# Performance work log

Measured on AMD Instinct MI355X. Metric: run time of the kernel, lower is better.

## Reference

```python
import jax, jax.numpy as jnp
import numpy as np

B, N, T, C = 16, 12, 128, 128  # batch, num_classes (nodes), temporal, channels


def _bn(x, gamma, beta, eps=1e-5):
    # BatchNorm2d in training mode: stats over (batch, t, c), channel axis 1, biased var
    mean = jnp.mean(x, axis=(0, 2, 3), keepdims=True)
    var = jnp.var(x, axis=(0, 2, 3), keepdims=True)
    xn = (x - mean) * jax.lax.rsqrt(var + eps)
    return xn * gamma[None, :, None, None] + beta[None, :, None, None]


def setup_inputs() -> dict:
    key = jax.random.key(0)
    ks = jax.random.split(key, 3)
    scale = np.float32(np.sqrt(2.0 / C))
    inp = {
        'x': jax.random.normal(ks[0], (B, N, T, C), dtype=jnp.float32),
        'edge': jax.random.normal(ks[1], (B, N * N, T, C), dtype=jnp.float32),
    }
    wk = jax.random.split(ks[2], 10)
    for name, k in zip(['A1', 'B1', 'E1', 'U1', 'V1', 'A2', 'B2', 'E2', 'U2', 'V2'], wk):
        inp[name] = jax.random.normal(k, (C, C), dtype=jnp.float32) * scale
    for name, dim in [('g_e1', N * N), ('b_e1', N * N), ('g_v1', N), ('b_v1', N),
                      ('g_e2', N * N), ('b_e2', N * N), ('g_v2', N), ('b_v2', N)]:
        inp[name] = jnp.ones((dim,), jnp.float32) if name[0] == 'g' else jnp.zeros((dim,), jnp.float32)
    return inp


def _forward(x, edge, A1, B1, E1, U1, V1, A2, B2, E2, U2, V2,
             g_e1, b_e1, g_v1, b_v1, g_e2, b_e2, g_v2, b_v2):
    # create_e_matrix: edge index e = i*N + j; 'end' selects node i, 'start' selects node j.
    # Dense incidence einsums become pure gathers; the transpose einsum is a
    # scatter-add over j, i.e. a reshape + sum.
    i_idx = jnp.repeat(jnp.arange(N), N)  # end-node of each edge
    j_idx = jnp.tile(jnp.arange(N), N)    # start-node of each edge
    b, _, t, c = x.shape

    def layer(x, edge, A, Bw, E, U, V, ge, be, gv, bv, mask_node):
        res = x
        edge_upd = (x @ A.T)[:, i_idx] + (x @ Bw.T)[:, j_idx] + edge @ E.T
        edge_upd = _bn(edge_upd, ge, be)
        edge_upd = jnp.where(jnp.isnan(edge_upd), 0.0, edge_upd)
        edge = edge + jax.nn.relu(edge_upd)
        e = jax.nn.sigmoid(edge)
        e = jax.nn.softmax(e.reshape(b, N, N, t, c), axis=2).reshape(b, N * N, t, c)
        Ujx = (x @ V.T)[:, j_idx]
        agg = (e * Ujx).reshape(b, N, N, t, c).sum(axis=2) / N  # scatter to end nodes
        xn = _bn(x @ U.T + agg, gv, bv)
        if mask_node:  # original only NaN-masks node BN in layer 1
            xn = jnp.where(jnp.isnan(xn), 0.0, xn)
        return jax.nn.relu(res + xn), edge

    x, edge = layer(x, edge, A1, B1, E1, U1, V1, g_e1, b_e1, g_v1, b_v1, True)
    x, edge = layer(x, edge, A2, B2, E2, U2, V2, g_e2, b_e2, g_v2, b_v2, False)
    return x, edge


def reference(x, edge, A1, B1, E1, U1, V1, A2, B2, E2, U2, V2,
              g_e1, b_e1, g_v1, b_v1, g_e2, b_e2, g_v2, b_v2):
    return _forward(x, edge, A1, B1, E1, U1, V1, A2, B2, E2, U2, V2,
                    g_e1, b_e1, g_v1, b_v1, g_e2, b_e2, g_v2, b_v2)
```

## Files before the change

kernel.cpp:

```cpp
#include <hip/hip_runtime.h>
#include <hip/hip_bf16.h>

#define BB 16
#define NN 12
#define NE 144
#define TT 128
#define CC 128

typedef __attribute__((ext_vector_type(8))) short v8s;
typedef __attribute__((ext_vector_type(4))) short v4s;
typedef __attribute__((ext_vector_type(4))) float v4f;

__device__ __forceinline__ short f2bf(float f) {
    unsigned u = __float_as_uint(f);
    u += 0x7fffu + ((u >> 16) & 1u);
    return (short)(u >> 16);
}
__device__ __forceinline__ float bf2f(unsigned short u) {
    return __uint_as_float(((unsigned)u) << 16);
}
__device__ __forceinline__ float rndbf(float f) { return bf2f((unsigned short)f2bf(f)); }
__device__ __forceinline__ v4s f4_to_bf4(float4 a) {
    v4s r; r[0] = f2bf(a.x); r[1] = f2bf(a.y); r[2] = f2bf(a.z); r[3] = f2bf(a.w); return r;
}

__global__ __launch_bounds__(256) void kW(
    const float* A1, const float* B1, const float* E1, const float* U1, const float* V1,
    const float* A2, const float* B2, const float* E2, const float* U2, const float* V2,
    unsigned short* wb)
{
    int idx = blockIdx.x * 256 + threadIdx.x;
    int w = idx >> 14, r = idx & 16383;
    const float* s;
    switch (w) {
        case 0: s = A1; break; case 1: s = B1; break; case 2: s = E1; break;
        case 3: s = U1; break; case 4: s = V1; break; case 5: s = A2; break;
        case 6: s = B2; break; case 7: s = E2; break; case 8: s = U2; break;
        default: s = V2; break;
    }
    wb[idx] = (unsigned short)f2bf(s[r]);
}

__global__ __launch_bounds__(256) void kP(
    const float* __restrict__ x, const unsigned short* __restrict__ wb,
    int sA, int sB, int sV, int sU,
    unsigned short* __restrict__ oA, unsigned short* __restrict__ oB,
    unsigned short* __restrict__ oV, unsigned short* __restrict__ oU)
{
    __shared__ unsigned short xt[64][136];
    int tid = threadIdx.x;
    int m0 = blockIdx.x * 64;
    #pragma unroll
    for (int it = 0; it < 8; ++it) {
        int f = it * 256 + tid;
        int row = f >> 5, c4 = f & 31;
        float4 v = *reinterpret_cast<const float4*>(x + (size_t)m0 * 128 + (size_t)f * 4);
        *reinterpret_cast<v4s*>(&xt[row][c4 * 4]) = f4_to_bf4(v);
    }
    __syncthreads();
    int lane = tid & 63, wid = tid >> 6;
    int l15 = lane & 15, l4 = lane >> 4;

    const unsigned short* Ws[4] = { wb + (size_t)sA * 16384, wb + (size_t)sB * 16384,
                                    wb + (size_t)sV * 16384, wb + (size_t)sU * 16384 };
    unsigned short* Os[4] = { oA, oB, oV, oU };

    #pragma unroll
    for (int w = 0; w < 4; ++w) {
        const unsigned short* W = Ws[w];
        unsigned short* out = Os[w];
        v8s bfr[2][4];
        #pragma unroll
        for (int nt2 = 0; nt2 < 2; ++nt2) {
            int col = (wid * 2 + nt2) * 16 + l15;
            #pragma unroll
            for (int kk = 0; kk < 4; ++kk)
                bfr[nt2][kk] = *reinterpret_cast<const v8s*>(W + col * 128 + kk * 32 + l4 * 8);
        }
        v4f acc[4][2] = {};
        #pragma unroll
        for (int kk = 0; kk < 4; ++kk) {
            #pragma unroll
            for (int mt = 0; mt < 4; ++mt) {
                v8s a = *reinterpret_cast<const v8s*>(&xt[mt * 16 + l15][kk * 32 + l4 * 8]);
                acc[mt][0] = __builtin_amdgcn_mfma_f32_16x16x32_bf16(a, bfr[0][kk], acc[mt][0], 0, 0, 0);
                acc[mt][1] = __builtin_amdgcn_mfma_f32_16x16x32_bf16(a, bfr[1][kk], acc[mt][1], 0, 0, 0);
            }
        }
        #pragma unroll
        for (int mt = 0; mt < 4; ++mt) {
            #pragma unroll
            for (int nt2 = 0; nt2 < 2; ++nt2) {
                int col = (wid * 2 + nt2) * 16 + l15;
                #pragma unroll
                for (int reg = 0; reg < 4; ++reg) {
                    int rowg = m0 + mt * 16 + l4 * 4 + reg;
                    out[(size_t)rowg * 128 + col] = (unsigned short)f2bf(acc[mt][nt2][reg]);
                }
            }
        }
    }
}

template<bool IN_F32>
__global__ __launch_bounds__(256, 4) void kA(
    const float* __restrict__ ef32, const unsigned short* __restrict__ ebf_in,
    unsigned short* __restrict__ ebf_out,
    const unsigned short* __restrict__ xAp, const unsigned short* __restrict__ xBp,
    const unsigned short* __restrict__ Ebf, float2* __restrict__ epart)
{
    __shared__ unsigned short et[64][136];
    __shared__ unsigned short xs[64][136];
    __shared__ float sblk[2];
    int tid = threadIdx.x;
    int bid = blockIdx.x;
    int th = bid & 1; int m = bid >> 1;
    int e = m % NE, b = m / NE;
    int iA = e / 12, jA = e - iA * 12;
    int t0 = th * 64;
    if (tid < 2) sblk[tid] = 0.f;
    size_t erow0 = ((size_t)(b * NE + e) * TT + t0) * CC;

    size_t xaoff = ((size_t)(b * NN + iA) * TT + t0) * CC;
    size_t xboff = ((size_t)(b * NN + jA) * TT + t0) * CC;
    #pragma unroll
    for (int it = 0; it < 4; ++it) {
        int f = it * 256 + tid;
        int row = f >> 4, c8 = f & 15;
        v8s xa = *reinterpret_cast<const v8s*>(xAp + xaoff + (size_t)row * CC + c8 * 8);
        v8s xb = *reinterpret_cast<const v8s*>(xBp + xboff + (size_t)row * CC + c8 * 8);
        v8s sv;
        #pragma unroll
        for (int k = 0; k < 8; ++k)
            sv[k] = f2bf(bf2f((unsigned short)xa[k]) + bf2f((unsigned short)xb[k]));
        *reinterpret_cast<v8s*>(&xs[row][c8 * 8]) = sv;
    }
    if constexpr (IN_F32) {
        #pragma unroll
        for (int it = 0; it < 8; ++it) {
            int f = it * 256 + tid;
            int row = f >> 5, c4 = f & 31;
            float4 v = *reinterpret_cast<const float4*>(ef32 + erow0 + (size_t)row * CC + c4 * 4);
            v4s bv = f4_to_bf4(v);
            *reinterpret_cast<v4s*>(&et[row][c4 * 4]) = bv;
            *reinterpret_cast<v4s*>(ebf_out + erow0 + (size_t)row * CC + c4 * 4) = bv;
        }
    } else {
        #pragma unroll
        for (int it = 0; it < 4; ++it) {
            int f = it * 256 + tid;
            int row = f >> 4, c8 = f & 15;
            *reinterpret_cast<v8s*>(&et[row][c8 * 8]) =
                *reinterpret_cast<const v8s*>(ebf_in + erow0 + (size_t)row * CC + c8 * 8);
        }
    }
    __syncthreads();

    int lane = tid & 63, wid = tid >> 6;
    int l15 = lane & 15, l4 = lane >> 4;

    v8s bfr[2][4];
    #pragma unroll
    for (int nt2 = 0; nt2 < 2; ++nt2) {
        int col = (wid * 2 + nt2) * 16 + l15;
        #pragma unroll
        for (int kk = 0; kk < 4; ++kk)
            bfr[nt2][kk] = *reinterpret_cast<const v8s*>(Ebf + col * 128 + kk * 32 + l4 * 8);
    }
    v4f acc[4][2] = {};
    #pragma unroll
    for (int kk = 0; kk < 4; ++kk) {
        #pragma unroll
        for (int mt = 0; mt < 4; ++mt) {
            v8s a = *reinterpret_cast<const v8s*>(&et[mt * 16 + l15][kk * 32 + l4 * 8]);
            acc[mt][0] = __builtin_amdgcn_mfma_f32_16x16x32_bf16(a, bfr[0][kk], acc[mt][0], 0, 0, 0);
            acc[mt][1] = __builtin_amdgcn_mfma_f32_16x16x32_bf16(a, bfr[1][kk], acc[mt][1], 0, 0, 0);
        }
    }
    float s = 0.f, q = 0.f;
    #pragma unroll
    for (int mt = 0; mt < 4; ++mt) {
        #pragma unroll
        for (int nt2 = 0; nt2 < 2; ++nt2) {
            int col = (wid * 2 + nt2) * 16 + l15;
            #pragma unroll
            for (int reg = 0; reg < 4; ++reg) {
                int row = mt * 16 + l4 * 4 + reg;
                float v = rndbf(acc[mt][nt2][reg]) + bf2f(xs[row][col]);
                s += v; q += v * v;
            }
        }
    }
    #pragma unroll
    for (int off = 1; off < 64; off <<= 1) { s += __shfl_xor(s, off); q += __shfl_xor(q, off); }
    if (lane == 0) { atomicAdd(&sblk[0], s); atomicAdd(&sblk[1], q); }
    __syncthreads();
    if (tid == 0) epart[bid] = make_float2(sblk[0], sblk[1]);
}

__global__ __launch_bounds__(64) void kRede(
    const float2* __restrict__ epart, const float* __restrict__ g,
    const float* __restrict__ be, float* __restrict__ estats)
{
    int e = blockIdx.x;
    int tid = threadIdx.x;
    float s = 0.f, q = 0.f;
    if (tid < 32) {
        int b = tid >> 1, th = tid & 1;
        float2 p = epart[(size_t)(b * NE + e) * 2 + th];
        s = p.x; q = p.y;
    }
    #pragma unroll
    for (int off = 1; off < 32; off <<= 1) { s += __shfl_xor(s, off); q += __shfl_xor(q, off); }
    if (tid == 0) {
        const float M = 262144.f;
        float mean = s / M;
        float var = q / M - mean * mean;
        float sc = g[e] * rsqrtf(var + 1e-5f);
        estats[e * 2] = sc;
        estats[e * 2 + 1] = be[e] - mean * sc;
    }
}

template<bool OUT_F32>
__global__ __launch_bounds__(256, 4) void kC(
    unsigned short* __restrict__ ebf,
    float* __restrict__ eout,
    const unsigned short* __restrict__ xAp, const unsigned short* __restrict__ xBp,
    const unsigned short* __restrict__ xV, const unsigned short* __restrict__ xU,
    const unsigned short* __restrict__ Ebf, const float* __restrict__ estats,
    unsigned short* __restrict__ yout, float* __restrict__ npart)
{
    __shared__ unsigned short et[48][136];
    __shared__ unsigned short xab[16][136];
    __shared__ unsigned short xv[12][136];
    __shared__ float2 scf[48];
    __shared__ float ns[4], nq[4];
    int tid = threadIdx.x;
    int bid = blockIdx.x;
    int third = bid % 3; int bt = bid / 3;
    int b = bt >> 7, t = bt & 127;
    if (tid < 48) scf[tid] = make_float2(estats[(third * 48 + tid) * 2],
                                         estats[(third * 48 + tid) * 2 + 1]);
    if (tid < 4) { ns[tid] = 0.f; nq[tid] = 0.f; }
    {
        int row = tid >> 4, c8 = tid & 15;
        const unsigned short* src = (row < 4)
            ? (xAp + (((size_t)(b * NN + third * 4 + row) * TT) + t) * CC)
            : (xBp + (((size_t)(b * NN + (row - 4)) * TT) + t) * CC);
        *reinterpret_cast<v8s*>(&xab[row][c8 * 8]) = *reinterpret_cast<const v8s*>(src + c8 * 8);
    }
    if (tid < 192) {
        int row = tid >> 4, c8 = tid & 15;
        *reinterpret_cast<v8s*>(&xv[row][c8 * 8]) =
            *reinterpret_cast<const v8s*>(xV + (((size_t)(b * NN + row) * TT) + t) * CC + c8 * 8);
    }
    #pragma unroll
    for (int it = 0; it < 3; ++it) {
        int f = it * 256 + tid;
        int row = f >> 4, c8 = f & 15;
        *reinterpret_cast<v8s*>(&et[row][c8 * 8]) =
            *reinterpret_cast<const v8s*>(ebf + (((size_t)(b * NE + third * 48 + row) * TT) + t) * CC + c8 * 8);
    }
    __syncthreads();
    int lane = tid & 63, wid = tid >> 6;
    int l15 = lane & 15, l4 = lane >> 4;

    v8s bfr[2][4];
    #pragma unroll
    for (int nt2 = 0; nt2 < 2; ++nt2) {
        int col = (wid * 2 + nt2) * 16 + l15;
        #pragma unroll
        for (int kk = 0; kk < 4; ++kk)
            bfr[nt2][kk] = *reinterpret_cast<const v8s*>(Ebf + col * 128 + kk * 32 + l4 * 8);
    }
    v4f acc[3][2] = {};
    #pragma unroll
    for (int kk = 0; kk < 4; ++kk) {
        #pragma unroll
        for (int mt = 0; mt < 3; ++mt) {
            v8s a = *reinterpret_cast<const v8s*>(&et[mt * 16 + l15][kk * 32 + l4 * 8]);
            acc[mt][0] = __builtin_amdgcn_mfma_f32_16x16x32_bf16(a, bfr[0][kk], acc[mt][0], 0, 0, 0);
            acc[mt][1] = __builtin_amdgcn_mfma_f32_16x16x32_bf16(a, bfr[1][kk], acc[mt][1], 0, 0, 0);
        }
    }
    __syncthreads();
    #pragma unroll
    for (int mt = 0; mt < 3; ++mt) {
        #pragma unroll
        for (int reg = 0; reg < 4; ++reg) {
            int r = mt * 16 + l4 * 4 + reg;
            int il = r / 12, jl = r - il * 12;
            float2 sc = scf[r];
            #pragma unroll
            for (int nt2 = 0; nt2 < 2; ++nt2) {
                int col = (wid * 2 + nt2) * 16 + l15;
                float upd = rndbf(acc[mt][nt2][reg]) + bf2f(xab[il][col]) + bf2f(xab[4 + jl][col]);
                float bn = fmaxf(sc.x * upd + sc.y, 0.f);
                float en = bf2f(et[r][col]) + bn;
                et[r][col] = (unsigned short)f2bf(en);
            }
        }
    }
    __syncthreads();
    #pragma unroll
    for (int it = 0; it < 3; ++it) {
        int f = it * 256 + tid;
        int row = f >> 4, c8 = f & 15;
        size_t goff = (((size_t)(b * NE + third * 48 + row) * TT) + t) * CC + c8 * 8;
        v8s nv = *reinterpret_cast<const v8s*>(&et[row][c8 * 8]);
        if constexpr (OUT_F32) {
            float4 o0, o1;
            o0.x = bf2f((unsigned short)nv[0]); o0.y = bf2f((unsigned short)nv[1]);
            o0.z = bf2f((unsigned short)nv[2]); o0.w = bf2f((unsigned short)nv[3]);
            o1.x = bf2f((unsigned short)nv[4]); o1.y = bf2f((unsigned short)nv[5]);
            o1.z = bf2f((unsigned short)nv[6]); o1.w = bf2f((unsigned short)nv[7]);
            *reinterpret_cast<float4*>(eout + goff)     = o0;
            *reinterpret_cast<float4*>(eout + goff + 4) = o1;
        } else {
            *reinterpret_cast<v8s*>(ebf + goff) = nv;
        }
    }
    #pragma unroll
    for (int ph = 0; ph < 2; ++ph) {
        int u = tid + ph * 256;
        int il = u >> 7, c = u & 127;
        float den = 0.f, ag = 0.f;
        #pragma unroll
        for (int j = 0; j < 12; ++j) {
            float sv = bf2f(et[il * 12 + j][c]);
            float sg = 1.f / (1.f + __expf(-sv));
            float ev = __expf(sg);
            den += ev;
            ag += ev * bf2f(xv[j][c]);
        }
        float agg = ag / (den * 12.f);
        int i = third * 4 + il;
        size_t xa = (((size_t)(b * NN + i) * TT) + t) * CC + c;
        float yv = bf2f(xU[xa]) + agg;
        unsigned short us = (unsigned short)f2bf(yv);
        yout[xa] = us;
        float yr = bf2f(us);
        float s1 = yr, s2 = yr * yr;
        #pragma unroll
        for (int off = 1; off < 64; off <<= 1) { s1 += __shfl_xor(s1, off); s2 += __shfl_xor(s2, off); }
        if (lane == 0) { atomicAdd(&ns[il], s1); atomicAdd(&nq[il], s2); }
    }
    __syncthreads();
    if (tid < 4) {
        npart[(size_t)bid * 8 + tid * 2 + 0] = ns[tid];
        npart[(size_t)bid * 8 + tid * 2 + 1] = nq[tid];
    }
}

__global__ __launch_bounds__(256) void kRedn(
    const float* __restrict__ npart, const float* __restrict__ g,
    const float* __restrict__ be, float* __restrict__ nstats)
{
    int n = blockIdx.x;
    int third = n >> 2, il = n & 3;
    float s = 0.f, q = 0.f;
    for (int bt = threadIdx.x; bt < 2048; bt += 256) {
        const float* p = npart + ((size_t)(bt * 3 + third) * 8 + il * 2);
        s += p[0]; q += p[1];
    }
    __shared__ float ss[4], qq[4];
    #pragma unroll
    for (int off = 32; off >= 1; off >>= 1) { s += __shfl_down(s, off); q += __shfl_down(q, off); }
    int wid = threadIdx.x >> 6;
    if ((threadIdx.x & 63) == 0) { ss[wid] = s; qq[wid] = q; }
    __syncthreads();
    if (threadIdx.x == 0) {
        s = ss[0] + ss[1] + ss[2] + ss[3];
        q = qq[0] + qq[1] + qq[2] + qq[3];
        const float M = 262144.f;
        float mean = s / M;
        float var = q / M - mean * mean;
        float sc = g[n] * rsqrtf(var + 1e-5f);
        nstats[n * 2] = sc;
        nstats[n * 2 + 1] = be[n] - mean * sc;
    }
}

__global__ __launch_bounds__(256) void kE(
    const float* xres, const unsigned short* __restrict__ yin,
    const float* __restrict__ nstats, float* xout)
{
    int idx4 = blockIdx.x * 256 + threadIdx.x;
    size_t base = (size_t)idx4 * 4;
    int n = (int)((base >> 14) % 12);
    float scv = nstats[n * 2], shv = nstats[n * 2 + 1];
    float4 xvv = *reinterpret_cast<const float4*>(xres + base);
    v4s yv4 = *reinterpret_cast<const v4s*>(yin + base);
    float4 o;
    o.x = fmaxf(xvv.x + scv * bf2f((unsigned short)yv4[0]) + shv, 0.f);
    o.y = fmaxf(xvv.y + scv * bf2f((unsigned short)yv4[1]) + shv, 0.f);
    o.z = fmaxf(xvv.z + scv * bf2f((unsigned short)yv4[2]) + shv, 0.f);
    o.w = fmaxf(xvv.w + scv * bf2f((unsigned short)yv4[3]) + shv, 0.f);
    *reinterpret_cast<float4*>(xout + base) = o;
}

extern "C" void kernel_launch(void* const* d_in, const int* in_sizes, int n_in,
                              void* d_out, int out_size, void* d_ws, size_t ws_size,
                              hipStream_t stream)
{
    const float* x0 = (const float*)d_in[0];
    const float* e0 = (const float*)d_in[1];
    const float* W[10];
    for (int i = 0; i < 10; ++i) W[i] = (const float*)d_in[2 + i];
    const float* ge1 = (const float*)d_in[12];
    const float* be1 = (const float*)d_in[13];
    const float* gv1 = (const float*)d_in[14];
    const float* bv1 = (const float*)d_in[15];
    const float* ge2 = (const float*)d_in[16];
    const float* be2 = (const float*)d_in[17];
    const float* gv2 = (const float*)d_in[18];
    const float* bv2 = (const float*)d_in[19];

    const size_t SZX = (size_t)BB * NN * TT * CC;
    const size_t SZE = (size_t)BB * NE * TT * CC;
    float* out_x = (float*)d_out;
    float* out_e = out_x + SZX;

    unsigned short* ws16 = (unsigned short*)d_ws;
    unsigned short* xA = ws16;
    unsigned short* xB = ws16 + SZX;
    unsigned short* xV = ws16 + 2 * SZX;
    unsigned short* xU = ws16 + 3 * SZX;
    unsigned short* yb = ws16 + 4 * SZX;
    unsigned short* ebf = ws16 + 5 * SZX;
    float2* epart  = (float2*)(ebf + SZE);
    float* estats = (float*)(epart + 4608);
    float* npart  = estats + 288;
    float* nstats = npart + 49152;
    unsigned short* wb = (unsigned short*)(nstats + 24);

    float* x1 = out_x;

    kW<<<640, 256, 0, stream>>>(W[0], W[1], W[2], W[3], W[4], W[5], W[6], W[7], W[8], W[9], wb);

    kP<<<384, 256, 0, stream>>>(x0, wb, 0, 1, 4, 3, xA, xB, xV, xU);
    kA<true><<<4608, 256, 0, stream>>>(e0, nullptr, ebf, xA, xB, wb + 2 * 16384, epart);
    kRede<<<144, 64, 0, stream>>>(epart, ge1, be1, estats);
    kC<false><<<6144, 256, 0, stream>>>(ebf, nullptr, xA, xB, xV, xU,
                                        wb + 2 * 16384, estats, yb, npart);
    kRedn<<<12, 256, 0, stream>>>(npart, gv1, bv1, nstats);
    kE<<<3072, 256, 0, stream>>>(x0, yb, nstats, x1);

    kP<<<384, 256, 0, stream>>>(x1, wb, 5, 6, 9, 8, xA, xB, xV, xU);
    kA<false><<<4608, 256, 0, stream>>>(nullptr, ebf, nullptr, xA, xB, wb + 7 * 16384, epart);
    kRede<<<144, 64, 0, stream>>>(epart, ge2, be2, estats);
    kC<true><<<6144, 256, 0, stream>>>(ebf, out_e, xA, xB, xV, xU,
                                       wb + 7 * 16384, estats, yb, npart);
    kRedn<<<12, 256, 0, stream>>>(npart, gv2, bv2, nstats);
    kE<<<3072, 256, 0, stream>>>(x1, yb, nstats, out_x);
}
```

Baseline: 275.8 us.

## Restructure edge stats kernel into independent per-wave tiles with global atomics

The first edge-update kernel now gives each wavefront its own 16-row time slice and its own LDS tile. Each wave computes all 8 output column tiles and fetches its weight fragments and the xA/xB node projections straight from global memory. This removes the block-level barriers, the shared staging of xA+xB and the per-block partial array. Per-edge sum and sum-of-squares are accumulated with global atomics into a buffer zeroed by the weight-conversion kernel, and the stats reducer is simplified to match. The trade-off is more repeated weight traffic per wave, scalar 2-byte gathers of the node projections, and atomic contention on each edge's pair of stat slots.

Result: slower. 407.7 us (+47.8%).

```diff
diff --git a/kernel.cpp b/kernel.cpp
--- a/kernel.cpp
+++ b/kernel.cpp
@@ -27,9 +27,10 @@
 __global__ __launch_bounds__(256) void kW(
     const float* A1, const float* B1, const float* E1, const float* U1, const float* V1,
     const float* A2, const float* B2, const float* E2, const float* U2, const float* V2,
-    unsigned short* wb)
+    unsigned short* wb, float* epzero)
 {
     int idx = blockIdx.x * 256 + threadIdx.x;
+    if (idx < 9216) epzero[idx] = 0.f;
     int w = idx >> 14, r = idx & 16383;
     const float* s;
     switch (w) {
@@ -107,111 +108,89 @@
     const float* __restrict__ ef32, const unsigned short* __restrict__ ebf_in,
     unsigned short* __restrict__ ebf_out,
     const unsigned short* __restrict__ xAp, const unsigned short* __restrict__ xBp,
-    const unsigned short* __restrict__ Ebf, float2* __restrict__ epart)
-{
-    __shared__ unsigned short et[64][136];
-    __shared__ unsigned short xs[64][136];
-    __shared__ float sblk[2];
+    const unsigned short* __restrict__ Ebf, float* __restrict__ epart)
+{
+    __shared__ unsigned short et[4][16][136];
     int tid = threadIdx.x;
-    int bid = blockIdx.x;
-    int th = bid & 1; int m = bid >> 1;
+    int wid = tid >> 6, lane = tid & 63;
+    int gwave = blockIdx.x * 4 + wid;
+    int tq = gwave & 7; int m = gwave >> 3;
     int e = m % NE, b = m / NE;
     int iA = e / 12, jA = e - iA * 12;
-    int t0 = th * 64;
-    if (tid < 2) sblk[tid] = 0.f;
+    int t0 = tq * 16;
     size_t erow0 = ((size_t)(b * NE + e) * TT + t0) * CC;
-
-    size_t xaoff = ((size_t)(b * NN + iA) * TT + t0) * CC;
-    size_t xboff = ((size_t)(b * NN + jA) * TT + t0) * CC;
-    #pragma unroll
-    for (int it = 0; it < 4; ++it) {
-        int f = it * 256 + tid;
-        int row = f >> 4, c8 = f & 15;
-        v8s xa = *reinterpret_cast<const v8s*>(xAp + xaoff + (size_t)row * CC + c8 * 8);
-        v8s xb = *reinterpret_cast<const v8s*>(xBp + xboff + (size_t)row * CC + c8 * 8);
-        v8s sv;
-        #pragma unroll
-        for (int k = 0; k < 8; ++k)
-            sv[k] = f2bf(bf2f((unsigned short)xa[k]) + bf2f((unsigned short)xb[k]));
-        *reinterpret_cast<v8s*>(&xs[row][c8 * 8]) = sv;
-    }
+    unsigned short (*myet)[136] = et[wid];
+
+    int srow = lane >> 4, c8 = lane & 15;
     if constexpr (IN_F32) {
         #pragma unroll
-        for (int it = 0; it < 8; ++it) {
-            int f = it * 256 + tid;
-            int row = f >> 5, c4 = f & 31;
-            float4 v = *reinterpret_cast<const float4*>(ef32 + erow0 + (size_t)row * CC + c4 * 4);
-            v4s bv = f4_to_bf4(v);
-            *reinterpret_cast<v4s*>(&et[row][c4 * 4]) = bv;
-            *reinterpret_cast<v4s*>(ebf_out + erow0 + (size_t)row * CC + c4 * 4) = bv;
+        for (int it = 0; it < 4; ++it) {
+            int row = srow + it * 4;
+            const float* p = ef32 + erow0 + (size_t)row * CC + c8 * 8;
+            float4 f0 = *reinterpret_cast<const float4*>(p);
+            float4 f1 = *reinterpret_cast<const float4*>(p + 4);
+            v8s bv;
+            bv[0] = f2bf(f0.x); bv[1] = f2bf(f0.y); bv[2] = f2bf(f0.z); bv[3] = f2bf(f0.w);
+            bv[4] = f2bf(f1.x); bv[5] = f2bf(f1.y); bv[6] = f2bf(f1.z); bv[7] = f2bf(f1.w);
+            *reinterpret_cast<v8s*>(&myet[row][c8 * 8]) = bv;
+            *reinterpret_cast<v8s*>(ebf_out + erow0 + (size_t)row * CC + c8 * 8) = bv;
         }
     } else {
         #pragma unroll
         for (int it = 0; it < 4; ++it) {
-            int f = it * 256 + tid;
-            int row = f >> 4, c8 = f & 15;
-            *reinterpret_cast<v8s*>(&et[row][c8 * 8]) =
+            int row = srow + it * 4;
+            *reinterpret_cast<v8s*>(&myet[row][c8 * 8]) =
                 *reinterpret_cast<const v8s*>(ebf_in + erow0 + (size_t)row * CC + c8 * 8);
         }
     }
-    __syncthreads();
-
-    int lane = tid & 63, wid = tid >> 6;
     int l15 = lane & 15, l4 = lane >> 4;
-
-    v8s bfr[2][4];
-    #pragma unroll
-    for (int nt2 = 0; nt2 < 2; ++nt2) {
-        int col = (wid * 2 + nt2) * 16 + l15;
-        #pragma unroll
-        for (int kk = 0; kk < 4; ++kk)
-            bfr[nt2][kk] = *reinterpret_cast<const v8s*>(Ebf + col * 128 + kk * 32 + l4 * 8);
-    }
-    v4f acc[4][2] = {};
-    #pragma unroll
-    for (int kk = 0; kk < 4; ++kk) {
-        #pragma unroll
-        for (int mt = 0; mt < 4; ++mt) {
-            v8s a = *reinterpret_cast<const v8s*>(&et[mt * 16 + l15][kk * 32 + l4 * 8]);
-            acc[mt][0] = __builtin_amdgcn_mfma_f32_16x16x32_bf16(a, bfr[0][kk], acc[mt][0], 0, 0, 0);
-            acc[mt][1] = __builtin_amdgcn_mfma_f32_16x16x32_bf16(a, bfr[1][kk], acc[mt][1], 0, 0, 0);
-        }
-    }
+    v8s af[4];
+    #pragma unroll
+    for (int kk = 0; kk < 4; ++kk)
+        af[kk] = *reinterpret_cast<const v8s*>(&myet[l15][kk * 32 + l4 * 8]);
+
+    size_t xabase = ((size_t)(b * NN + iA) * TT + t0) * CC;
+    size_t xbbase = ((size_t)(b * NN + jA) * TT + t0) * CC;
     float s = 0.f, q = 0.f;
     #pragma unroll
-    for (int mt = 0; mt < 4; ++mt) {
-        #pragma unroll
-        for (int nt2 = 0; nt2 < 2; ++nt2) {
-            int col = (wid * 2 + nt2) * 16 + l15;
-            #pragma unroll
-            for (int reg = 0; reg < 4; ++reg) {
-                int row = mt * 16 + l4 * 4 + reg;
-                float v = rndbf(acc[mt][nt2][reg]) + bf2f(xs[row][col]);
-                s += v; q += v * v;
-            }
+    for (int nt = 0; nt < 8; ++nt) {
+        int col = nt * 16 + l15;
+        v4f acc = {};
+        #pragma unroll
+        for (int kk = 0; kk < 4; ++kk) {
+            v8s bf = *reinterpret_cast<const v8s*>(Ebf + (size_t)col * 128 + kk * 32 + l4 * 8);
+            acc = __builtin_amdgcn_mfma_f32_16x16x32_bf16(af[kk], bf, acc, 0, 0, 0);
+        }
+        #pragma unroll
+        for (int reg = 0; reg < 4; ++reg) {
+            int trow = l4 * 4 + reg;
+            float xaf = bf2f(xAp[xabase + (size_t)trow * CC + col]);
+            float xbf = bf2f(xBp[xbbase + (size_t)trow * CC + col]);
+            float v = acc[reg] + xaf + xbf;
+            s += v; q += v * v;
         }
     }
     #pragma unroll
     for (int off = 1; off < 64; off <<= 1) { s += __shfl_xor(s, off); q += __shfl_xor(q, off); }
-    if (lane == 0) { atomicAdd(&sblk[0], s); atomicAdd(&sblk[1], q); }
-    __syncthreads();
-    if (tid == 0) epart[bid] = make_float2(sblk[0], sblk[1]);
+    if (lane == 0) {
+        atomicAdd(&epart[(size_t)(b * NE + e) * 2 + 0], s);
+        atomicAdd(&epart[(size_t)(b * NE + e) * 2 + 1], q);
+    }
 }
 
 __global__ __launch_bounds__(64) void kRede(
-    const float2* __restrict__ epart, const float* __restrict__ g,
+    const float* __restrict__ epart, const float* __restrict__ g,
     const float* __restrict__ be, float* __restrict__ estats)
 {
     int e = blockIdx.x;
     int tid = threadIdx.x;
     float s = 0.f, q = 0.f;
-    if (tid < 32) {
-        int b = tid >> 1, th = tid & 1;
-        float2 p = epart[(size_t)(b * NE + e) * 2 + th];
-        s = p.x; q = p.y;
-    }
-    #pragma unroll
-    for (int off = 1; off < 32; off <<= 1) { s += __shfl_xor(s, off); q += __shfl_xor(q, off); }
+    if (tid < 16) {
+        s = epart[(size_t)(tid * NE + e) * 2 + 0];
+        q = epart[(size_t)(tid * NE + e) * 2 + 1];
+    }
+    #pragma unroll
+    for (int off = 1; off < 16; off <<= 1) { s += __shfl_xor(s, off); q += __shfl_xor(q, off); }
     if (tid == 0) {
         const float M = 262144.f;
         float mean = s / M;
@@ -429,27 +408,31 @@
     unsigned short* xU = ws16 + 3 * SZX;
     unsigned short* yb = ws16 + 4 * SZX;
     unsigned short* ebf = ws16 + 5 * SZX;
-    float2* epart  = (float2*)(ebf + SZE);
-    float* estats = (float*)(epart + 4608);
+    float* epart  = (float*)(ebf + SZE);
+    float* estats = epart + 9216;
     float* npart  = estats + 288;
     float* nstats = npart + 49152;
     unsigned short* wb = (unsigned short*)(nstats + 24);
 
+    float* epart1 = epart;
+    float* epart2 = epart + 4608;
+
     float* x1 = out_x;
 
-    kW<<<640, 256, 0, stream>>>(W[0], W[1], W[2], W[3], W[4], W[5], W[6], W[7], W[8], W[9], wb);
+    kW<<<640, 256, 0, stream>>>(W[0], W[1], W[2], W[3], W[4], W[5], W[6], W[7], W[8], W[9],
+                                wb, epart);
 
     kP<<<384, 256, 0, stream>>>(x0, wb, 0, 1, 4, 3, xA, xB, xV, xU);
-    kA<true><<<4608, 256, 0, stream>>>(e0, nullptr, ebf, xA, xB, wb + 2 * 16384, epart);
-    kRede<<<144, 64, 0, stream>>>(epart, ge1, be1, estats);
+    kA<true><<<4608, 256, 0, stream>>>(e0, nullptr, ebf, xA, xB, wb + 2 * 16384, epart1);
+    kRede<<<144, 64, 0, stream>>>(epart1, ge1, be1, estats);
     kC<false><<<6144, 256, 0, stream>>>(ebf, nullptr, xA, xB, xV, xU,
                                         wb + 2 * 16384, estats, yb, npart);
     kRedn<<<12, 256, 0, stream>>>(npart, gv1, bv1, nstats);
     kE<<<3072, 256, 0, stream>>>(x0, yb, nstats, x1);
 
     kP<<<384, 256, 0, stream>>>(x1, wb, 5, 6, 9, 8, xA, xB, xV, xU);
-    kA<false><<<4608, 256, 0, stream>>>(nullptr, ebf, nullptr, xA, xB, wb + 7 * 16384, epart);
-    kRede<<<144, 64, 0, stream>>>(epart, ge2, be2, estats);
+    kA<false><<<4608, 256, 0, stream>>>(nullptr, ebf, nullptr, xA, xB, wb + 7 * 16384, epart2);
+    kRede<<<144, 64, 0, stream>>>(epart2, ge2, be2, estats);
     kC<true><<<6144, 256, 0, stream>>>(ebf, out_e, xA, xB, xV, xU,
                                        wb + 7 * 16384, estats, yb, npart);
     kRedn<<<12, 256, 0, stream>>>(npart, gv2, bv2, nstats);
```
